# Optimization experiments

Measured on AMD Instinct MI355X. Metric: run time of the kernel, lower is better.

The kernel has to match this reference:

```python
import jax, jax.numpy as jnp
import numpy as np

B, S, H, D = 2, 2048, 16, 128
HID = H * D  # 2048


def _quantum(x, real, imag, phase, mag):
    # |x * e^{i*phase} * (real + i*imag) * mag| == |x| * sqrt(real^2+imag^2) * |mag|
    # (phase has unit modulus, so it drops out of the magnitude; grad wrt phase is 0,
    # matching torch.abs of the complex product.)
    return jnp.abs(x) * jnp.sqrt(real * real + imag * imag) * jnp.abs(mag)


def setup_inputs() -> dict:
    key = jax.random.key(0)
    ks = jax.random.split(key, 20)
    p = lambda i, shape, s=0.02: jax.random.normal(ks[i], shape, dtype=jnp.float32) * s
    inp = {
        "hidden_states": jax.random.normal(ks[0], (B, S, HID), dtype=jnp.float32),
        "attention_mask": jnp.zeros((B, 1, 1, S), dtype=jnp.float32),
    }
    i = 1
    for name in ("q", "k", "v"):
        inp[name + "_real"] = p(i, (HID,)); i += 1
        inp[name + "_imag"] = p(i, (HID,)); i += 1
        inp[name + "_phase"] = p(i, (HID,), 0.1); i += 1
        inp[name + "_mag"] = jnp.ones((HID,), dtype=jnp.float32)
    for name in ("q", "k", "v", "o"):
        inp["W" + name] = p(i, (HID, HID)); i += 1  # torch Linear weight [out, in]
        inp["b" + name] = jnp.zeros((HID,), dtype=jnp.float32)
    inp["ent"] = p(i, (H, H))
    return inp


def reference(hidden_states, attention_mask,
              q_real, q_imag, q_phase, q_mag,
              k_real, k_imag, k_phase, k_mag,
              v_real, v_imag, v_phase, v_mag,
              Wq, bq, Wk, bk, Wv, bv, Wo, bo, ent):
    Bsz, Sl, _ = hidden_states.shape

    def heads(x):  # [B,S,HID] -> [B,H,S,D]
        return x.reshape(Bsz, Sl, H, D).transpose(0, 2, 1, 3)

    q = heads(_quantum(hidden_states @ Wq.T + bq, q_real, q_imag, q_phase, q_mag))
    k = heads(_quantum(hidden_states @ Wk.T + bk, k_real, k_imag, k_phase, k_mag))
    v = heads(_quantum(hidden_states @ Wv.T + bv, v_real, v_imag, v_phase, v_mag))

    scores = jnp.einsum('bhsd,bhtd->bhst', q, k) / jnp.sqrt(jnp.float32(D))
    # entanglement bias: [H,H] tiled along key axis -> [1,H,1,S]
    bias = jnp.tile(ent, (1, Sl // H))[None, :, None, :]
    scores = scores + bias + attention_mask
    probs = jax.nn.softmax(scores, axis=-1)

    ctx = jnp.einsum('bhst,bhtd->bhsd', probs, v)
    ctx = ctx.transpose(0, 2, 1, 3).reshape(Bsz, Sl, HID)
    return ctx @ Wo.T + bo
```

## Files before the change

kernel.cpp:

```cpp
#include <hip/hip_runtime.h>
#include <hip/hip_bf16.h>

#define NB 2
#define NS 2048
#define NH 16
#define ND 128
#define HID2 2048
#define MROWS 4096

typedef __bf16 bf16;
typedef bf16 bf16x8 __attribute__((ext_vector_type(8)));
typedef bf16 bf16x4 __attribute__((ext_vector_type(4)));
typedef float f32x4 __attribute__((ext_vector_type(4)));
typedef unsigned int u32;

#define GLOBAL_AS __attribute__((address_space(1)))
#define LDS_AS __attribute__((address_space(3)))

__device__ __forceinline__ void async16(void* lds, const void* g) {
    __builtin_amdgcn_global_load_lds((const GLOBAL_AS u32*)g, (LDS_AS u32*)lds, 16, 0, 0);
}

__global__ void cvt_f32_bf16(const float* __restrict__ src, bf16* __restrict__ dst, int n8) {
    int i = blockIdx.x * blockDim.x + threadIdx.x;
    if (i >= n8) return;
    const float4* s4 = (const float4*)src;
    float4 a = s4[2 * i], b = s4[2 * i + 1];
    bf16x8 o;
    o[0] = (bf16)a.x; o[1] = (bf16)a.y; o[2] = (bf16)a.z; o[3] = (bf16)a.w;
    o[4] = (bf16)b.x; o[5] = (bf16)b.y; o[6] = (bf16)b.z; o[7] = (bf16)b.w;
    ((bf16x8*)dst)[i] = o;
}

__global__ void qscale_kernel(const float* qr, const float* qi, const float* qm,
                              const float* kr, const float* ki, const float* km,
                              const float* vr, const float* vi, const float* vm,
                              float* out) {
    int i = blockIdx.x * blockDim.x + threadIdx.x;
    if (i >= HID2) return;
    out[i]            = sqrtf(qr[i] * qr[i] + qi[i] * qi[i]) * fabsf(qm[i]);
    out[HID2 + i]     = sqrtf(kr[i] * kr[i] + ki[i] * ki[i]) * fabsf(km[i]);
    out[2 * HID2 + i] = sqrtf(vr[i] * vr[i] + vi[i] * vi[i]) * fabsf(vm[i]);
}

template <int MODE>
__device__ __forceinline__ void gemm_core(const bf16* __restrict__ A, const bf16* __restrict__ Bt,
                                          const float* __restrict__ bias, const float* __restrict__ scale,
                                          void* __restrict__ Cout, int tm, int tn) {
    __shared__ bf16 At[128 * 64];
    __shared__ bf16 Bs[128 * 64];
    const int K = HID2;
    int tid = threadIdx.x;
    int wid = tid >> 6, lane = tid & 63;
    int wr = wid >> 1, wc = wid & 1;
    int l15 = lane & 15, l4 = lane >> 4;
    int rowA0 = tm * 128, rowB0 = tn * 128;

    const bf16* gA = A + (size_t)(rowA0 + wid * 8 + (lane >> 3)) * K + (lane & 7) * 8;
    const bf16* gB = Bt + (size_t)(rowB0 + wid * 8 + (lane >> 3)) * K + (lane & 7) * 8;
    char* lA = (char*)At + wid * 8 * 128;
    char* lB = (char*)Bs + wid * 8 * 128;

    f32x4 acc[4][4] = {};

    for (int k0 = 0; k0 < K; k0 += 64) {
#pragma unroll
        for (int c = 0; c < 4; ++c) {
            async16(lA + c * 32 * 128, gA + (size_t)(c * 32) * K + k0);
            async16(lB + c * 32 * 128, gB + (size_t)(c * 32) * K + k0);
        }
        __syncthreads();
#pragma unroll
        for (int kk = 0; kk < 64; kk += 32) {
            bf16x8 af[4], bfr[4];
#pragma unroll
            for (int m = 0; m < 4; ++m)
                af[m] = *(const bf16x8*)(At + (wr * 64 + m * 16 + l15) * 64 + kk + l4 * 8);
#pragma unroll
            for (int n = 0; n < 4; ++n)
                bfr[n] = *(const bf16x8*)(Bs + (wc * 64 + n * 16 + l15) * 64 + kk + l4 * 8);
#pragma unroll
            for (int m = 0; m < 4; ++m)
#pragma unroll
                for (int n = 0; n < 4; ++n)
                    acc[m][n] = __builtin_amdgcn_mfma_f32_16x16x32_bf16(af[m], bfr[n], acc[m][n], 0, 0, 0);
        }
        __syncthreads();
    }

#pragma unroll
    for (int m = 0; m < 4; ++m) {
        int row = rowA0 + wr * 64 + m * 16 + l4 * 4;
#pragma unroll
        for (int n = 0; n < 4; ++n) {
            int col = rowB0 + wc * 64 + n * 16 + l15;
            float bv = bias[col];
            if (MODE == 0) {
                float sc = scale[col];
                bf16* Cp = (bf16*)Cout;
#pragma unroll
                for (int r = 0; r < 4; ++r)
                    Cp[(size_t)(row + r) * HID2 + col] = (bf16)(fabsf(acc[m][n][r] + bv) * sc);
            } else {
                float* Cp = (float*)Cout;
#pragma unroll
                for (int r = 0; r < 4; ++r)
                    Cp[(size_t)(row + r) * HID2 + col] = acc[m][n][r] + bv;
            }
        }
    }
}

__global__ __launch_bounds__(256, 2) void gemm_qkv_kernel(
    const bf16* __restrict__ X, const bf16* __restrict__ Wb,
    const float* __restrict__ bq, const float* __restrict__ bk, const float* __restrict__ bv,
    const float* __restrict__ scales, bf16* __restrict__ QKV) {
    int z = blockIdx.y;
    int tile = blockIdx.x;
    const bf16* W = Wb + (size_t)z * HID2 * HID2;
    const float* bias = (z == 0) ? bq : (z == 1) ? bk : bv;
    const float* scale = scales + z * HID2;
    bf16* out = QKV + (size_t)z * MROWS * HID2;
    gemm_core<0>(X, W, bias, scale, out, tile >> 4, tile & 15);
}

__global__ __launch_bounds__(256, 2) void gemm_out_kernel(
    const bf16* __restrict__ Ctx, const bf16* __restrict__ Wo,
    const float* __restrict__ bo, float* __restrict__ out) {
    int tile = blockIdx.x;
    gemm_core<1>(Ctx, Wo, bo, nullptr, out, tile >> 4, tile & 15);
}

__global__ void transpose_v(const bf16* __restrict__ Vb, bf16* __restrict__ Vt) {
    int bh = blockIdx.z;
    int b = bh >> 4, h = bh & 15;
    int s0 = blockIdx.x * 64, d0 = blockIdx.y * 64;
    int tid = threadIdx.x;
    __shared__ bf16 T[64][72];
    const bf16* src = Vb + ((size_t)b * NS + s0) * HID2 + h * ND + d0;
#pragma unroll
    for (int i = 0; i < 2; ++i) {
        int r = i * 32 + (tid >> 3);
        int c = (tid & 7) * 8;
        *(bf16x8*)(&T[r][c]) = *(const bf16x8*)(src + (size_t)r * HID2 + c);
    }
    __syncthreads();
    bf16* dst = Vt + ((size_t)(b * NH + h) * ND + d0) * NS + s0;
#pragma unroll
    for (int i = 0; i < 2; ++i) {
        int dr = i * 32 + (tid >> 3);
        int sc = (tid & 7) * 8;
        bf16x8 o;
#pragma unroll
        for (int j = 0; j < 8; ++j) o[j] = T[sc + j][dr];
        *(bf16x8*)(dst + (size_t)dr * NS + sc) = o;
    }
}

__device__ __forceinline__ void stage_load(const bf16* __restrict__ Kp, const bf16* __restrict__ Vp,
                                           int kt, int tid, bf16x8 kreg[4], bf16x8 vreg[4]) {
#pragma unroll
    for (int i = 0; i < 4; ++i) {
        kreg[i] = *(const bf16x8*)(Kp + (size_t)(kt * 64 + i * 16 + (tid >> 4)) * HID2 + (tid & 15) * 8);
        vreg[i] = *(const bf16x8*)(Vp + (size_t)(i * 32 + (tid >> 3)) * NS + kt * 64 + (tid & 7) * 8);
    }
}

__global__ __launch_bounds__(256, 2) void flash_kernel(
    const bf16* __restrict__ Qb, const bf16* __restrict__ Kb, const bf16* __restrict__ Vt,
    const float* __restrict__ ent, const float* __restrict__ mask, bf16* __restrict__ Ctx) {
    int qt = blockIdx.x;
    int bh = blockIdx.y;
    int b = bh >> 4, h = bh & 15;
    int tid = threadIdx.x, wid = tid >> 6, lane = tid & 63;
    int l15 = lane & 15, l4 = lane >> 4;

    __shared__ bf16 Ks[64 * 136];
    __shared__ bf16 Vs[128 * 72];
    __shared__ bf16 Ps[4][32 * 72];

    const bf16* Qp = Qb + ((size_t)b * NS + qt * 128) * HID2 + h * ND;
    const bf16* Kp = Kb + (size_t)b * NS * HID2 + h * ND;
    const bf16* Vp = Vt + (size_t)(b * NH + h) * ND * NS;
    const float* maskp = mask + (size_t)b * NS;

    bf16x8 qf[2][4];
#pragma unroll
    for (int m = 0; m < 2; ++m)
#pragma unroll
        for (int kk = 0; kk < 4; ++kk)
            qf[m][kk] = *(const bf16x8*)(Qp + (size_t)(wid * 32 + m * 16 + l15) * HID2 + kk * 32 + l4 * 8);

    float eb[4];
#pragma unroll
    for (int r = 0; r < 4; ++r) eb[r] = ent[h * NH + l4 * 4 + r];
    const float RSQD = 0.08838834764831845f;

    float mrun[2], lrun[2];
    mrun[0] = mrun[1] = -INFINITY;
    lrun[0] = lrun[1] = 0.f;
    f32x4 oacc[2][8] = {};

    bf16x8 kreg[4], vreg[4];
    stage_load(Kp, Vp, 0, tid, kreg, vreg);
#pragma unroll
    for (int i = 0; i < 4; ++i) {
        *(bf16x8*)(&Ks[(i * 16 + (tid >> 4)) * 136 + (tid & 15) * 8]) = kreg[i];
        *(bf16x8*)(&Vs[(i * 32 + (tid >> 3)) * 72 + (tid & 7) * 8]) = vreg[i];
    }

    for (int kt = 0; kt < NS / 64; ++kt) {
        __syncthreads();
        if (kt + 1 < NS / 64) stage_load(Kp, Vp, kt + 1, tid, kreg, vreg);

        f32x4 s[2][4] = {};
#pragma unroll
        for (int kk = 0; kk < 4; ++kk) {
            bf16x8 kf[4];
#pragma unroll
            for (int n = 0; n < 4; ++n)
                kf[n] = *(const bf16x8*)(&Ks[(n * 16 + l15) * 136 + kk * 32 + l4 * 8]);
#pragma unroll
            for (int m = 0; m < 2; ++m)
#pragma unroll
                for (int n = 0; n < 4; ++n)
                    s[m][n] = __builtin_amdgcn_mfma_f32_16x16x32_bf16(kf[n], qf[m][kk], s[m][n], 0, 0, 0);
        }

        float4 mk[4];
#pragma unroll
        for (int n = 0; n < 4; ++n)
            mk[n] = *(const float4*)(maskp + kt * 64 + n * 16 + l4 * 4);

#pragma unroll
        for (int mq = 0; mq < 2; ++mq) {
            float sv[4][4];
#pragma unroll
            for (int n = 0; n < 4; ++n) {
                sv[n][0] = s[mq][n][0] * RSQD + eb[0] + mk[n].x;
                sv[n][1] = s[mq][n][1] * RSQD + eb[1] + mk[n].y;
                sv[n][2] = s[mq][n][2] * RSQD + eb[2] + mk[n].z;
                sv[n][3] = s[mq][n][3] * RSQD + eb[3] + mk[n].w;
            }
            float tmax = sv[0][0];
#pragma unroll
            for (int n = 0; n < 4; ++n)
#pragma unroll
                for (int r = 0; r < 4; ++r) tmax = fmaxf(tmax, sv[n][r]);
            tmax = fmaxf(tmax, __shfl_xor(tmax, 16));
            tmax = fmaxf(tmax, __shfl_xor(tmax, 32));

            if (__any(tmax > mrun[mq] + 8.0f)) {
                float mnew = fmaxf(mrun[mq], tmax);
                float corr = __expf(mrun[mq] - mnew);
                mrun[mq] = mnew;
                lrun[mq] *= corr;
#pragma unroll
                for (int r = 0; r < 4; ++r) {
                    float cr = __shfl(corr, l4 * 4 + r);
#pragma unroll
                    for (int n = 0; n < 8; ++n) oacc[mq][n][r] *= cr;
                }
            }

            float psum = 0.f;
#pragma unroll
            for (int n = 0; n < 4; ++n) {
                bf16x4 pv;
#pragma unroll
                for (int r = 0; r < 4; ++r) {
                    float p = __expf(sv[n][r] - mrun[mq]);
                    psum += p;
                    pv[r] = (bf16)p;
                }
                *(bf16x4*)(&Ps[wid][(mq * 16 + l15) * 72 + n * 16 + l4 * 4]) = pv;
            }
            psum += __shfl_xor(psum, 16);
            psum += __shfl_xor(psum, 32);
            lrun[mq] += psum;
        }

#pragma unroll
        for (int kk = 0; kk < 2; ++kk) {
            bf16x8 pa[2], vb[8];
#pragma unroll
            for (int m = 0; m < 2; ++m)
                pa[m] = *(const bf16x8*)(&Ps[wid][(m * 16 + l15) * 72 + kk * 32 + l4 * 8]);
#pragma unroll
            for (int n = 0; n < 8; ++n)
                vb[n] = *(const bf16x8*)(&Vs[(n * 16 + l15) * 72 + kk * 32 + l4 * 8]);
#pragma unroll
            for (int m = 0; m < 2; ++m)
#pragma unroll
                for (int n = 0; n < 8; ++n)
                    oacc[m][n] = __builtin_amdgcn_mfma_f32_16x16x32_bf16(pa[m], vb[n], oacc[m][n], 0, 0, 0);
        }
        __syncthreads();
        if (kt + 1 < NS / 64) {
#pragma unroll
            for (int i = 0; i < 4; ++i) {
                *(bf16x8*)(&Ks[(i * 16 + (tid >> 4)) * 136 + (tid & 15) * 8]) = kreg[i];
                *(bf16x8*)(&Vs[(i * 32 + (tid >> 3)) * 72 + (tid & 7) * 8]) = vreg[i];
            }
        }
    }

#pragma unroll
    for (int m = 0; m < 2; ++m) {
        float inv = 1.0f / lrun[m];
        float invr[4];
#pragma unroll
        for (int r = 0; r < 4; ++r) invr[r] = __shfl(inv, l4 * 4 + r);
#pragma unroll
        for (int r = 0; r < 4; ++r) {
            int row = qt * 128 + wid * 32 + m * 16 + l4 * 4 + r;
            bf16* Cp = Ctx + ((size_t)b * NS + row) * HID2 + h * ND;
#pragma unroll
            for (int n = 0; n < 8; ++n)
                Cp[n * 16 + l15] = (bf16)(oacc[m][n][r] * invr[r]);
        }
    }
}

extern "C" void kernel_launch(void* const* d_in, const int* in_sizes, int n_in,
                              void* d_out, int out_size, void* d_ws, size_t ws_size,
                              hipStream_t stream) {
    const float* hidden = (const float*)d_in[0];
    const float* mask   = (const float*)d_in[1];
    const float* q_real = (const float*)d_in[2];
    const float* q_imag = (const float*)d_in[3];
    const float* q_mag  = (const float*)d_in[5];
    const float* k_real = (const float*)d_in[6];
    const float* k_imag = (const float*)d_in[7];
    const float* k_mag  = (const float*)d_in[9];
    const float* v_real = (const float*)d_in[10];
    const float* v_imag = (const float*)d_in[11];
    const float* v_mag  = (const float*)d_in[13];
    const float* Wq = (const float*)d_in[14];
    const float* bq = (const float*)d_in[15];
    const float* Wk = (const float*)d_in[16];
    const float* bk = (const float*)d_in[17];
    const float* Wv = (const float*)d_in[18];
    const float* bv = (const float*)d_in[19];
    const float* Wo = (const float*)d_in[20];
    const float* bo = (const float*)d_in[21];
    const float* ent = (const float*)d_in[22];

    char* ws = (char*)d_ws;
    bf16* Xb    = (bf16*)(ws);
    bf16* Wb    = (bf16*)(ws + 16777216);
    bf16* Wob   = (bf16*)(ws + 41943040);
    bf16* QKV   = (bf16*)(ws + 50331648);
    bf16* Vt    = (bf16*)(ws + 100663296);
    bf16* Ctx   = (bf16*)(ws + 117440512);
    float* scales = (float*)(ws + 134217728);

    const int W8 = HID2 * HID2 / 8;

    cvt_f32_bf16<<<4096, 256, 0, stream>>>(hidden, Xb, MROWS * HID2 / 8);
    cvt_f32_bf16<<<2048, 256, 0, stream>>>(Wq, Wb, W8);
    cvt_f32_bf16<<<2048, 256, 0, stream>>>(Wk, Wb + (size_t)HID2 * HID2, W8);
    cvt_f32_bf16<<<2048, 256, 0, stream>>>(Wv, Wb + (size_t)2 * HID2 * HID2, W8);
    cvt_f32_bf16<<<2048, 256, 0, stream>>>(Wo, Wob, W8);
    qscale_kernel<<<8, 256, 0, stream>>>(q_real, q_imag, q_mag, k_real, k_imag, k_mag,
                                         v_real, v_imag, v_mag, scales);
    gemm_qkv_kernel<<<dim3(512, 3), 256, 0, stream>>>(Xb, Wb, bq, bk, bv, scales, QKV);
    const bf16* Vb = QKV + (size_t)2 * MROWS * HID2;
    transpose_v<<<dim3(32, 2, 32), 256, 0, stream>>>(Vb, Vt);
    flash_kernel<<<dim3(16, 32), 256, 0, stream>>>(QKV, QKV + (size_t)MROWS * HID2, Vt, ent, mask, Ctx);
    gemm_out_kernel<<<512, 256, 0, stream>>>(Ctx, Wob, bo, (float*)d_out);
}
```

Before: 299.3 us.

## Rewrite GEMMs as 8-wave 128x256 tiles with triple-buffered swizzled LDS pipeline

Replaces the single-buffered 128x128 GEMM core with an 8-wave, 128x256 tile kernel that stages K-tiles into a 3-deep LDS ring through async global-to-LDS loads two steps ahead. LDS rows are XOR-swizzled to avoid bank conflicts, and MFMA phases are bracketed with barriers and setprio so that loads overlap compute. The intent is to hide global memory latency and raise MFMA utilisation in the QKV and output projections. The cost is much more LDS per block (about 144KB), which limits occupancy, plus hand-tuned vmcnt waits that must match the number of issued loads exactly.

```diff
diff --git a/kernel.cpp b/kernel.cpp
--- a/kernel.cpp
+++ b/kernel.cpp
@@ -43,60 +43,101 @@
     out[2 * HID2 + i] = sqrtf(vr[i] * vr[i] + vi[i] * vi[i]) * fabsf(vm[i]);
 }
 
+__device__ __forceinline__ void stage6(const char* gA, const char* gB,
+                                       char* sa, char* sb, int w, int lane) {
+#pragma unroll
+    for (int j = 0; j < 2; ++j) {
+        int r = w * 16 + j * 8 + (lane >> 3);
+        async16(sa + (w * 16 + j * 8) * 128,
+                gA + (size_t)r * (HID2 * 2) + (((lane & 7) * 16) ^ ((r & 12) << 3)));
+    }
+#pragma unroll
+    for (int j = 0; j < 4; ++j) {
+        int r = w * 32 + j * 8 + (lane >> 3);
+        async16(sb + (w * 32 + j * 8) * 128,
+                gB + (size_t)r * (HID2 * 2) + (((lane & 7) * 16) ^ ((r & 12) << 3)));
+    }
+}
+
 template <int MODE>
-__device__ __forceinline__ void gemm_core(const bf16* __restrict__ A, const bf16* __restrict__ Bt,
-                                          const float* __restrict__ bias, const float* __restrict__ scale,
-                                          void* __restrict__ Cout, int tm, int tn) {
-    __shared__ bf16 At[128 * 64];
-    __shared__ bf16 Bs[128 * 64];
-    const int K = HID2;
-    int tid = threadIdx.x;
-    int wid = tid >> 6, lane = tid & 63;
-    int wr = wid >> 1, wc = wid & 1;
+__device__ __forceinline__ void gemm8_core(const bf16* __restrict__ A, const bf16* __restrict__ Bt,
+                                           const float* __restrict__ bias, const float* __restrict__ scale,
+                                           void* __restrict__ Cout, int tm, int tn) {
+    __shared__ bf16 sA[3][128 * 64];
+    __shared__ bf16 sB[3][256 * 64];
+    const int NT = HID2 / 64;
+    int tid = threadIdx.x, w = tid >> 6, lane = tid & 63;
+    int wr = w >> 2, wc = w & 3;
     int l15 = lane & 15, l4 = lane >> 4;
-    int rowA0 = tm * 128, rowB0 = tn * 128;
-
-    const bf16* gA = A + (size_t)(rowA0 + wid * 8 + (lane >> 3)) * K + (lane & 7) * 8;
-    const bf16* gB = Bt + (size_t)(rowB0 + wid * 8 + (lane >> 3)) * K + (lane & 7) * 8;
-    char* lA = (char*)At + wid * 8 * 128;
-    char* lB = (char*)Bs + wid * 8 * 128;
+    int xorb = (l15 & 12) << 3;
+
+    const char* gAb = (const char*)(A + (size_t)tm * 128 * HID2);
+    const char* gBb = (const char*)(Bt + (size_t)tn * 256 * HID2);
 
     f32x4 acc[4][4] = {};
 
-    for (int k0 = 0; k0 < K; k0 += 64) {
-#pragma unroll
-        for (int c = 0; c < 4; ++c) {
-            async16(lA + c * 32 * 128, gA + (size_t)(c * 32) * K + k0);
-            async16(lB + c * 32 * 128, gB + (size_t)(c * 32) * K + k0);
-        }
-        __syncthreads();
-#pragma unroll
-        for (int kk = 0; kk < 64; kk += 32) {
-            bf16x8 af[4], bfr[4];
-#pragma unroll
-            for (int m = 0; m < 4; ++m)
-                af[m] = *(const bf16x8*)(At + (wr * 64 + m * 16 + l15) * 64 + kk + l4 * 8);
+    stage6(gAb, gBb, (char*)sA[0], (char*)sB[0], w, lane);
+    stage6(gAb + 128, gBb + 128, (char*)sA[1], (char*)sB[1], w, lane);
+    asm volatile("s_waitcnt vmcnt(6)" ::: "memory");
+    __builtin_amdgcn_s_barrier();
+
+    for (int t = 0; t < NT; ++t) {
+        int cur = t - (t / 3) * 3;
+        const char* pa = (const char*)sA[cur];
+        const char* pb = (const char*)sB[cur];
+        if (t + 2 < NT) {
+            int nb = (t + 2) - ((t + 2) / 3) * 3;
+            stage6(gAb + (size_t)(t + 2) * 128, gBb + (size_t)(t + 2) * 128,
+                   (char*)sA[nb], (char*)sB[nb], w, lane);
+        }
+        bf16x8 af[4], bg[4];
+#pragma unroll
+        for (int m = 0; m < 4; ++m)
+            af[m] = *(const bf16x8*)(pa + (wr * 64 + m * 16 + l15) * 128 + ((l4 * 16) ^ xorb));
+#pragma unroll
+        for (int n = 0; n < 4; ++n)
+            bg[n] = *(const bf16x8*)(pb + (wc * 64 + n * 16 + l15) * 128 + ((l4 * 16) ^ xorb));
+        __builtin_amdgcn_s_barrier();
+        asm volatile("s_waitcnt lgkmcnt(0)" ::: "memory");
+        __builtin_amdgcn_sched_barrier(0);
+        __builtin_amdgcn_s_setprio(1);
+#pragma unroll
+        for (int m = 0; m < 4; ++m)
 #pragma unroll
             for (int n = 0; n < 4; ++n)
-                bfr[n] = *(const bf16x8*)(Bs + (wc * 64 + n * 16 + l15) * 64 + kk + l4 * 8);
-#pragma unroll
-            for (int m = 0; m < 4; ++m)
-#pragma unroll
-                for (int n = 0; n < 4; ++n)
-                    acc[m][n] = __builtin_amdgcn_mfma_f32_16x16x32_bf16(af[m], bfr[n], acc[m][n], 0, 0, 0);
-        }
-        __syncthreads();
-    }
-
-#pragma unroll
-    for (int m = 0; m < 4; ++m) {
-        int row = rowA0 + wr * 64 + m * 16 + l4 * 4;
-#pragma unroll
-        for (int n = 0; n < 4; ++n) {
-            int col = rowB0 + wc * 64 + n * 16 + l15;
-            float bv = bias[col];
+                acc[m][n] = __builtin_amdgcn_mfma_f32_16x16x32_bf16(af[m], bg[n], acc[m][n], 0, 0, 0);
+        __builtin_amdgcn_s_setprio(0);
+        __builtin_amdgcn_s_barrier();
+#pragma unroll
+        for (int m = 0; m < 4; ++m)
+            af[m] = *(const bf16x8*)(pa + (wr * 64 + m * 16 + l15) * 128 + ((64 + l4 * 16) ^ xorb));
+#pragma unroll
+        for (int n = 0; n < 4; ++n)
+            bg[n] = *(const bf16x8*)(pb + (wc * 64 + n * 16 + l15) * 128 + ((64 + l4 * 16) ^ xorb));
+        __builtin_amdgcn_s_barrier();
+        asm volatile("s_waitcnt lgkmcnt(0)" ::: "memory");
+        __builtin_amdgcn_sched_barrier(0);
+        __builtin_amdgcn_s_setprio(1);
+#pragma unroll
+        for (int m = 0; m < 4; ++m)
+#pragma unroll
+            for (int n = 0; n < 4; ++n)
+                acc[m][n] = __builtin_amdgcn_mfma_f32_16x16x32_bf16(af[m], bg[n], acc[m][n], 0, 0, 0);
+        __builtin_amdgcn_s_setprio(0);
+        if (t + 2 < NT)      { asm volatile("s_waitcnt vmcnt(6)" ::: "memory"); }
+        else if (t + 1 < NT) { asm volatile("s_waitcnt vmcnt(0)" ::: "memory"); }
+        __builtin_amdgcn_s_barrier();
+    }
+
+#pragma unroll
+    for (int n = 0; n < 4; ++n) {
+        int col = tn * 256 + wc * 64 + n * 16 + l15;
+        float bv = bias[col];
+        float sc = (MODE == 0) ? scale[col] : 0.f;
+#pragma unroll
+        for (int m = 0; m < 4; ++m) {
+            int row = tm * 128 + wr * 64 + m * 16 + l4 * 4;
             if (MODE == 0) {
-                float sc = scale[col];
                 bf16* Cp = (bf16*)Cout;
 #pragma unroll
                 for (int r = 0; r < 4; ++r)
@@ -111,24 +152,24 @@
     }
 }
 
-__global__ __launch_bounds__(256, 2) void gemm_qkv_kernel(
+__global__ __launch_bounds__(512, 2) void gemm8_qkv(
     const bf16* __restrict__ X, const bf16* __restrict__ Wb,
     const float* __restrict__ bq, const float* __restrict__ bk, const float* __restrict__ bv,
     const float* __restrict__ scales, bf16* __restrict__ QKV) {
     int z = blockIdx.y;
-    int tile = blockIdx.x;
+    int bid = blockIdx.x;
+    int tn = bid & 7, tm = bid >> 3;
     const bf16* W = Wb + (size_t)z * HID2 * HID2;
     const float* bias = (z == 0) ? bq : (z == 1) ? bk : bv;
-    const float* scale = scales + z * HID2;
-    bf16* out = QKV + (size_t)z * MROWS * HID2;
-    gemm_core<0>(X, W, bias, scale, out, tile >> 4, tile & 15);
-}
-
-__global__ __launch_bounds__(256, 2) void gemm_out_kernel(
+    gemm8_core<0>(X, W, bias, scales + z * HID2, QKV + (size_t)z * MROWS * HID2, tm, tn);
+}
+
+__global__ __launch_bounds__(512, 2) void gemm8_out(
     const bf16* __restrict__ Ctx, const bf16* __restrict__ Wo,
     const float* __restrict__ bo, float* __restrict__ out) {
-    int tile = blockIdx.x;
-    gemm_core<1>(Ctx, Wo, bo, nullptr, out, tile >> 4, tile & 15);
+    int bid = blockIdx.x;
+    int tn = bid & 7, tm = bid >> 3;
+    gemm8_core<1>(Ctx, Wo, bo, nullptr, out, tm, tn);
 }
 
 __global__ void transpose_v(const bf16* __restrict__ Vb, bf16* __restrict__ Vt) {
@@ -364,9 +405,9 @@
     cvt_f32_bf16<<<2048, 256, 0, stream>>>(Wo, Wob, W8);
     qscale_kernel<<<8, 256, 0, stream>>>(q_real, q_imag, q_mag, k_real, k_imag, k_mag,
                                          v_real, v_imag, v_mag, scales);
-    gemm_qkv_kernel<<<dim3(512, 3), 256, 0, stream>>>(Xb, Wb, bq, bk, bv, scales, QKV);
+    gemm8_qkv<<<dim3(256, 3), 512, 0, stream>>>(Xb, Wb, bq, bk, bv, scales, QKV);
     const bf16* Vb = QKV + (size_t)2 * MROWS * HID2;
     transpose_v<<<dim3(32, 2, 32), 256, 0, stream>>>(Vb, Vt);
     flash_kernel<<<dim3(16, 32), 256, 0, stream>>>(QKV, QKV + (size_t)MROWS * HID2, Vt, ent, mask, Ctx);
-    gemm_out_kernel<<<512, 256, 0, stream>>>(Ctx, Wob, bo, (float*)d_out);
-}
+    gemm8_out<<<256, 512, 0, stream>>>(Ctx, Wob, bo, (float*)d_out);
+}
```

After: 371.7 us. +24.2%, slower.
